# Performance work log

Measured on AMD Instinct MI355X. Metric: run time of the kernel, lower is better.

Reference implementation:

```python
import jax, jax.numpy as jnp
import numpy as np

S, B, D, H = 2048, 2, 1024, 16
DK = D // H


def setup_inputs() -> dict:
    key = jax.random.key(0)
    k1, k2, k3 = jax.random.split(key, 3)
    x = jax.random.normal(k1, (S, B, D), dtype=jnp.float32)
    # xavier-uniform-like scale for weights
    w_qkv = jax.random.normal(k2, (3 * D, D), dtype=jnp.float32) * (1.0 / np.sqrt(D))
    w_out = jax.random.normal(k3, (D, D), dtype=jnp.float32) * (1.0 / np.sqrt(D))
    b_out = jnp.zeros((D,), dtype=jnp.float32)
    return {"x": x, "w_qkv": w_qkv, "w_out": w_out, "b_out": b_out}


def reference(x, w_qkv, w_out, b_out):
    seq_len, batch, d_model = x.shape
    n_heads = H
    d_k = d_model // n_heads
    # qkv projection: [S,B,3D]
    qkv = jnp.einsum('sbd,ed->sbe', x, w_qkv)
    qkv = qkv.reshape(seq_len, batch, 3, n_heads, d_k)
    qkv = jnp.transpose(qkv, (2, 1, 3, 0, 4))  # [3,B,H,S,dk]
    q, k, v = qkv[0], qkv[1], qkv[2]
    scores = jnp.einsum('bhqd,bhkd->bhqk', q, k) / jnp.sqrt(jnp.asarray(d_k, x.dtype))
    causal = jnp.triu(jnp.ones((seq_len, seq_len), dtype=bool), k=1)
    scores = jnp.where(causal[None, None], jnp.asarray(-jnp.inf, scores.dtype), scores)
    weights = jax.nn.softmax(scores, axis=-1)
    out = jnp.einsum('bhqk,bhkd->bhqd', weights, v)  # [B,H,S,dk]
    out = jnp.transpose(out, (2, 0, 1, 3)).reshape(seq_len, batch, d_model)
    return jnp.einsum('sbd,ed->sbe', out, w_out) + b_out
```

## Files before the change

### kernel.cpp

```cpp
#include <hip/hip_runtime.h>
#include <cstdint>

typedef _Float16 f16;
typedef _Float16 f16x4 __attribute__((ext_vector_type(4)));
typedef _Float16 f16x8 __attribute__((ext_vector_type(8)));
typedef float f32x4 __attribute__((ext_vector_type(4)));

#define MFMA16(a, b, c) __builtin_amdgcn_mfma_f32_16x16x32_f16(a, b, c, 0, 0, 0)
#define QSCALE 0.1803368801111243f

__device__ __forceinline__ void gload_lds16(const void* g, void* l) {
    __builtin_amdgcn_global_load_lds((__attribute__((address_space(1))) void*)(g),
                                     (__attribute__((address_space(3))) void*)(l),
                                     16, 0, 0);
}


__global__ void cast_all(const float* __restrict__ x, const float* __restrict__ wqv,
                         const float* __restrict__ wo, f16* __restrict__ out) {
    int i = blockIdx.x * blockDim.x + threadIdx.x;
    const float* src; int li;
    if (i < 1048576)      { src = x;   li = i; }
    else if (i < 1835008) { src = wqv; li = i - 1048576; }
    else                  { src = wo;  li = i - 1835008; }
    float4 v = reinterpret_cast<const float4*>(src)[li];
    f16x4 o = {(f16)v.x, (f16)v.y, (f16)v.z, (f16)v.w};
    reinterpret_cast<f16x4*>(out)[i] = o;
}

__global__ __launch_bounds__(256) void gemm_qkv(
    const f16* __restrict__ A, const f16* __restrict__ B,
    f16* __restrict__ outq, f16* __restrict__ outk, f16* __restrict__ outvt)
{
    __shared__ f16 SM[128 * 64 * 2];
    f16* As = SM;
    f16* Bs = SM + 8192;
    const int tid = threadIdx.x;
    const int lane = tid & 63;
    const int wave = tid >> 6;
    const int wm = wave >> 1, wn = wave & 1;
    const int bm = blockIdx.y * 128, bn = blockIdx.x * 128;
    const int sr = tid >> 3;
    const int scu = (tid & 7) ^ (sr & 7);
    const int fr = lane & 15, fq = lane >> 4;
    const int u0 = (fq ^ (fr & 7)) * 8;
    const int u1 = ((4 + fq) ^ (fr & 7)) * 8;

    f32x4 acc[4][4] = {};

    for (int k0 = 0; k0 < 1024; k0 += 64) {
        __syncthreads();
#pragma unroll
        for (int is = 0; is < 4; ++is) {
            gload_lds16(&A[(bm + sr + is * 32) * 1024 + k0 + scu * 8], &As[is * 2048 + tid * 8]);
            gload_lds16(&B[(bn + sr + is * 32) * 1024 + k0 + scu * 8], &Bs[is * 2048 + tid * 8]);
        }
        __syncthreads();
        f16x8 af0[4], af1[4], bf0[4], bf1[4];
#pragma unroll
        for (int mt = 0; mt < 4; ++mt) {
            int r = wm * 64 + mt * 16 + fr;
            af0[mt] = *(const f16x8*)&As[r * 64 + u0];
            af1[mt] = *(const f16x8*)&As[r * 64 + u1];
        }
#pragma unroll
        for (int nt = 0; nt < 4; ++nt) {
            int r = wn * 64 + nt * 16 + fr;
            bf0[nt] = *(const f16x8*)&Bs[r * 64 + u0];
            bf1[nt] = *(const f16x8*)&Bs[r * 64 + u1];
        }
#pragma unroll
        for (int mt = 0; mt < 4; ++mt)
#pragma unroll
            for (int nt = 0; nt < 4; ++nt) {
                acc[mt][nt] = MFMA16(af0[mt], bf0[nt], acc[mt][nt]);
                acc[mt][nt] = MFMA16(af1[mt], bf1[nt], acc[mt][nt]);
            }
    }

    const int x = blockIdx.x;
    if (x < 16) {
        f16* base = (x < 8) ? outq : outk;
        const float scale = (x < 8) ? QSCALE : 1.0f;
        const int coloff = (x < 8) ? bn : (bn - 1024);
#pragma unroll
        for (int mt = 0; mt < 4; ++mt)
#pragma unroll
            for (int nt = 0; nt < 4; ++nt)
#pragma unroll
                for (int i = 0; i < 4; ++i) {
                    int row = bm + wm * 64 + mt * 16 + fq * 4 + i;
                    int col = coloff + wn * 64 + nt * 16 + fr;
                    int s = row >> 1, b = row & 1;
                    int h = col >> 6, dk = col & 63;
                    base[((b * 16 + h) * 2048 + s) * 64 + dk] = (f16)(acc[mt][nt][i] * scale);
                }
    } else {
        const int xb = x - 16;
        const int s0 = bm >> 1;
        f16* Ts = SM;
#pragma unroll
        for (int p = 0; p < 2; ++p) {
            __syncthreads();
            if (wn == p) {
#pragma unroll
                for (int mt = 0; mt < 4; ++mt)
#pragma unroll
                    for (int nt = 0; nt < 4; ++nt)
#pragma unroll
                        for (int i = 0; i < 4; ++i) {
                            int row = wm * 64 + mt * 16 + fq * 4 + i;
                            int cl = nt * 16 + fr;
                            Ts[(cl * 2 + (row & 1)) * 76 + (row >> 1)] = (f16)acc[mt][nt][i];
                        }
            }
            __syncthreads();
            const int h = xb * 2 + p;
            const int sj = tid & 7;
#pragma unroll
            for (int it = 0; it < 4; ++it) {
                int idx = (tid >> 3) + it * 32;
                int bsel = idx & 1, dk = idx >> 1;
                f16x8 v = *(const f16x8*)&Ts[(dk * 2 + bsel) * 76 + sj * 8];
                *(f16x8*)&outvt[((bsel * 16 + h) * 64 + dk) * 2048 + s0 + sj * 8] = v;
            }
        }
    }
}

__global__ __launch_bounds__(256) void attn_kernel(
    const f16* __restrict__ qg, const f16* __restrict__ kg,
    const f16* __restrict__ vtg, f16* __restrict__ attn)
{
    __shared__ f16 Ks[2][64 * 64];
    __shared__ f16 Vs[2][64 * 64];
    __shared__ f16 plds[4][16 * 72];
    const int tid = threadIdx.x;
    const int lane = tid & 63;
    const int wave = tid >> 6;
    const int qpair = blockIdx.x;
    const int bh = blockIdx.y;
    const int b = bh >> 4, h = bh & 15;
    const int fr = lane & 15, fq = lane >> 4;

    const int bqA = qpair * 64;
    const int bqB = (31 - qpair) * 64;
    const int nA = qpair + 1;
    const int nB = 32 - qpair;
    const int qrowA = bqA + wave * 16;
    const int qrowB = bqB + wave * 16;

    const f16* Q  = qg  + bh * 2048 * 64;
    const f16* K  = kg  + bh * 2048 * 64;
    const f16* VT = vtg + bh * 64 * 2048;
    f16* P = plds[wave];

    const int sr = tid >> 3;
    const int scu = (tid & 7) ^ (sr & 7);

    f16x8 aqA0 = *(const f16x8*)&Q[(qrowA + fr) * 64 + fq * 8];
    f16x8 aqA1 = *(const f16x8*)&Q[(qrowA + fr) * 64 + 32 + fq * 8];
    f16x8 aqB0 = *(const f16x8*)&Q[(qrowB + fr) * 64 + fq * 8];
    f16x8 aqB1 = *(const f16x8*)&Q[(qrowB + fr) * 64 + 32 + fq * 8];

    f32x4 oA[4] = {}, oB[4] = {};
    float lA[4] = {}, lB[4] = {};

    auto stage = [&](int kc, int buf) {
        const int kb = kc * 64;
        gload_lds16(&K[(kb + sr) * 64 + scu * 8],         &Ks[buf][tid * 8]);
        gload_lds16(&K[(kb + sr + 32) * 64 + scu * 8],    &Ks[buf][2048 + tid * 8]);
        gload_lds16(&VT[sr * 2048 + kb + scu * 8],        &Vs[buf][tid * 8]);
        gload_lds16(&VT[(sr + 32) * 2048 + kb + scu * 8], &Vs[buf][2048 + tid * 8]);
    };

    auto compute = [&](const f16x8& aq0, const f16x8& aq1, int qrow0, int kb,
                       const f16* Ksb, const f16* Vsb, f32x4* oacc, float* li, bool domask) {
        f32x4 sc[4] = {};
#pragma unroll
        for (int ct = 0; ct < 4; ++ct) {
            int r = ct * 16 + fr;
            f16x8 b0 = *(const f16x8*)&Ksb[r * 64 + ((fq ^ (r & 7)) * 8)];
            f16x8 b1 = *(const f16x8*)&Ksb[r * 64 + (((4 + fq) ^ (r & 7)) * 8)];
            sc[ct] = MFMA16(aq0, b0, sc[ct]);
            sc[ct] = MFMA16(aq1, b1, sc[ct]);
        }
        if (domask) {
#pragma unroll
            for (int ct = 0; ct < 4; ++ct) {
                int kcol = kb + ct * 16 + fr;
#pragma unroll
                for (int i = 0; i < 4; ++i)
                    if (kcol > qrow0 + fq * 4 + i) sc[ct][i] = -1e30f;
            }
        }
#pragma unroll
        for (int i = 0; i < 4; ++i) {
            float p0 = __builtin_amdgcn_exp2f(sc[0][i]);
            float p1 = __builtin_amdgcn_exp2f(sc[1][i]);
            float p2 = __builtin_amdgcn_exp2f(sc[2][i]);
            float p3 = __builtin_amdgcn_exp2f(sc[3][i]);
            li[i] += (p0 + p1) + (p2 + p3);
            P[(fq * 4 + i) * 72 + fr]      = (f16)p0;
            P[(fq * 4 + i) * 72 + 16 + fr] = (f16)p1;
            P[(fq * 4 + i) * 72 + 32 + fr] = (f16)p2;
            P[(fq * 4 + i) * 72 + 48 + fr] = (f16)p3;
        }
        f16x8 ap0 = *(const f16x8*)&P[fr * 72 + fq * 8];
        f16x8 ap1 = *(const f16x8*)&P[fr * 72 + 32 + fq * 8];
#pragma unroll
        for (int nt = 0; nt < 4; ++nt) {
            int dk = nt * 16 + fr;
            f16x8 bv0 = *(const f16x8*)&Vsb[dk * 64 + ((fq ^ (dk & 7)) * 8)];
            f16x8 bv1 = *(const f16x8*)&Vsb[dk * 64 + (((4 + fq) ^ (dk & 7)) * 8)];
            oacc[nt] = MFMA16(ap0, bv0, oacc[nt]);
            oacc[nt] = MFMA16(ap1, bv1, oacc[nt]);
        }
    };

    stage(0, 0);
    for (int kc = 0; kc < nB; ++kc) {
        const int kb = kc * 64;
        const int cur = kc & 1;
        __syncthreads();
        if (kc + 1 < nB) stage(kc + 1, cur ^ 1);
        compute(aqB0, aqB1, qrowB, kb, Ks[cur], Vs[cur], oB, lB, kb + 63 > qrowB);
        if (kc < nA)
            compute(aqA0, aqA1, qrowA, kb, Ks[cur], Vs[cur], oA, lA, kb + 63 > qrowA);
    }

#pragma unroll
    for (int i = 0; i < 4; ++i) {
        float rs = lA[i];
        rs += __shfl_xor(rs, 1);
        rs += __shfl_xor(rs, 2);
        rs += __shfl_xor(rs, 4);
        rs += __shfl_xor(rs, 8);
        float inv = __builtin_amdgcn_rcpf(rs);
        int srow = qrowA + fq * 4 + i;
#pragma unroll
        for (int nt = 0; nt < 4; ++nt)
            attn[(srow * 2 + b) * 1024 + h * 64 + nt * 16 + fr] = (f16)(oA[nt][i] * inv);
    }
#pragma unroll
    for (int i = 0; i < 4; ++i) {
        float rs = lB[i];
        rs += __shfl_xor(rs, 1);
        rs += __shfl_xor(rs, 2);
        rs += __shfl_xor(rs, 4);
        rs += __shfl_xor(rs, 8);
        float inv = __builtin_amdgcn_rcpf(rs);
        int srow = qrowB + fq * 4 + i;
#pragma unroll
        for (int nt = 0; nt < 4; ++nt)
            attn[(srow * 2 + b) * 1024 + h * 64 + nt * 16 + fr] = (f16)(oB[nt][i] * inv);
    }
}

__global__ __launch_bounds__(256) void gemm_out(
    const f16* __restrict__ A, const f16* __restrict__ B,
    const float* __restrict__ bias, float* __restrict__ out)
{
    __shared__ f16 As[128 * 64];
    __shared__ f16 Bs[64 * 64];
    const int tid = threadIdx.x;
    const int lane = tid & 63;
    const int wave = tid >> 6;
    const int wm = wave >> 1, wn = wave & 1;
    const int bm = blockIdx.y * 128, bn = blockIdx.x * 64;
    const int sr = tid >> 3;
    const int scu = (tid & 7) ^ (sr & 7);
    const int fr = lane & 15, fq = lane >> 4;
    const int u0 = (fq ^ (fr & 7)) * 8;
    const int u1 = ((4 + fq) ^ (fr & 7)) * 8;

    f32x4 acc[4][2] = {};

    for (int k0 = 0; k0 < 1024; k0 += 64) {
        __syncthreads();
#pragma unroll
        for (int is = 0; is < 4; ++is)
            gload_lds16(&A[(bm + sr + is * 32) * 1024 + k0 + scu * 8], &As[is * 2048 + tid * 8]);
#pragma unroll
        for (int is = 0; is < 2; ++is)
            gload_lds16(&B[(bn + sr + is * 32) * 1024 + k0 + scu * 8], &Bs[is * 2048 + tid * 8]);
        __syncthreads();
        f16x8 af0[4], af1[4], bf0[2], bf1[2];
#pragma unroll
        for (int mt = 0; mt < 4; ++mt) {
            int r = wm * 64 + mt * 16 + fr;
            af0[mt] = *(const f16x8*)&As[r * 64 + u0];
            af1[mt] = *(const f16x8*)&As[r * 64 + u1];
        }
#pragma unroll
        for (int nt = 0; nt < 2; ++nt) {
            int r = wn * 32 + nt * 16 + fr;
            bf0[nt] = *(const f16x8*)&Bs[r * 64 + u0];
            bf1[nt] = *(const f16x8*)&Bs[r * 64 + u1];
        }
#pragma unroll
        for (int mt = 0; mt < 4; ++mt)
#pragma unroll
            for (int nt = 0; nt < 2; ++nt) {
                acc[mt][nt] = MFMA16(af0[mt], bf0[nt], acc[mt][nt]);
                acc[mt][nt] = MFMA16(af1[mt], bf1[nt], acc[mt][nt]);
            }
    }

#pragma unroll
    for (int mt = 0; mt < 4; ++mt)
#pragma unroll
        for (int nt = 0; nt < 2; ++nt)
#pragma unroll
            for (int i = 0; i < 4; ++i) {
                int row = bm + wm * 64 + mt * 16 + fq * 4 + i;
                int col = bn + wn * 32 + nt * 16 + fr;
                out[row * 1024 + col] = acc[mt][nt][i] + bias[col];
            }
}

extern "C" void kernel_launch(void* const* d_in, const int* in_sizes, int n_in,
                              void* d_out, int out_size, void* d_ws, size_t ws_size,
                              hipStream_t stream)
{
    const float* x     = (const float*)d_in[0];
    const float* w_qkv = (const float*)d_in[1];
    const float* w_out = (const float*)d_in[2];
    const float* b_out = (const float*)d_in[3];
    float* out = (float*)d_out;

    char* ws = (char*)d_ws;
    f16* xh  = (f16*)(ws);
    f16* wqh = (f16*)(ws + 8388608);
    f16* woh = (f16*)(ws + 14680064);
    f16* qh  = (f16*)(ws + 16777216);
    f16* kh  = (f16*)(ws + 25165824);
    f16* vt  = (f16*)(ws + 33554432);
    f16* ah  = (f16*)(ws + 41943040);

    cast_all<<<8192, 256, 0, stream>>>(x, w_qkv, w_out, xh);
    gemm_qkv<<<dim3(24, 32), 256, 0, stream>>>(xh, wqh, qh, kh, vt);
    attn_kernel<<<dim3(16, 32), 256, 0, stream>>>(qh, kh, vt, ah);
    gemm_out<<<dim3(16, 32), 256, 0, stream>>>(ah, woh, b_out, out);
}
```

Measured before the change: 185.8 us.

## Split attention key range in two halves and merge with a combine kernel

The attention grid is doubled by splitting each query-pair's key loop into two halves. Each half writes unnormalized partial outputs and row sums to separate buffers in reused workspace. A new combine kernel then adds the partials and normalizes them. A constant table reorders block indices so the heavier halves are scheduled first. The aim is more parallelism and better load balance across CUs, at the cost of an extra kernel launch, extra global traffic, and unnormalized fp16 intermediates.

```diff
diff --git a/kernel.cpp b/kernel.cpp
--- a/kernel.cpp
+++ b/kernel.cpp
@@ -128,9 +128,14 @@
     }
 }
 
+__device__ __constant__ const unsigned char ATTN_ORDER[32] = {
+    18,20,22,14,16,10,12,24,26,6,8,2,4,28,30,0,
+    1,3,5,29,31,7,9,11,13,25,27,15,17,19,21,23};
+
 __global__ __launch_bounds__(256) void attn_kernel(
     const f16* __restrict__ qg, const f16* __restrict__ kg,
-    const f16* __restrict__ vtg, f16* __restrict__ attn)
+    const f16* __restrict__ vtg, f16* __restrict__ Op0, f16* __restrict__ Op1,
+    float* __restrict__ lp0, float* __restrict__ lp1)
 {
     __shared__ f16 Ks[2][64 * 64];
     __shared__ f16 Vs[2][64 * 64];
@@ -138,7 +143,9 @@
     const int tid = threadIdx.x;
     const int lane = tid & 63;
     const int wave = tid >> 6;
-    const int qpair = blockIdx.x;
+    const int enc = ATTN_ORDER[blockIdx.x];
+    const int qpair = enc >> 1;
+    const int half = enc & 1;
     const int bh = blockIdx.y;
     const int b = bh >> 4, h = bh & 15;
     const int fr = lane & 15, fq = lane >> 4;
@@ -147,6 +154,9 @@
     const int bqB = (31 - qpair) * 64;
     const int nA = qpair + 1;
     const int nB = 32 - qpair;
+    const int h0 = (nB + 1) >> 1;
+    const int k0 = half ? h0 : 0;
+    const int k1 = half ? nB : h0;
     const int qrowA = bqA + wave * 16;
     const int qrowB = bqB + wave * 16;
 
@@ -218,17 +228,19 @@
         }
     };
 
-    stage(0, 0);
-    for (int kc = 0; kc < nB; ++kc) {
+    stage(k0, k0 & 1);
+    for (int kc = k0; kc < k1; ++kc) {
         const int kb = kc * 64;
         const int cur = kc & 1;
         __syncthreads();
-        if (kc + 1 < nB) stage(kc + 1, cur ^ 1);
+        if (kc + 1 < k1) stage(kc + 1, cur ^ 1);
         compute(aqB0, aqB1, qrowB, kb, Ks[cur], Vs[cur], oB, lB, kb + 63 > qrowB);
         if (kc < nA)
             compute(aqA0, aqA1, qrowA, kb, Ks[cur], Vs[cur], oA, lA, kb + 63 > qrowA);
     }
 
+    f16* Op = half ? Op1 : Op0;
+    float* lp = half ? lp1 : lp0;
 #pragma unroll
     for (int i = 0; i < 4; ++i) {
         float rs = lA[i];
@@ -236,11 +248,11 @@
         rs += __shfl_xor(rs, 2);
         rs += __shfl_xor(rs, 4);
         rs += __shfl_xor(rs, 8);
-        float inv = __builtin_amdgcn_rcpf(rs);
         int srow = qrowA + fq * 4 + i;
+        if (fr == 0) lp[(srow * 2 + b) * 16 + h] = rs;
 #pragma unroll
         for (int nt = 0; nt < 4; ++nt)
-            attn[(srow * 2 + b) * 1024 + h * 64 + nt * 16 + fr] = (f16)(oA[nt][i] * inv);
+            Op[(srow * 2 + b) * 1024 + h * 64 + nt * 16 + fr] = (f16)oA[nt][i];
     }
 #pragma unroll
     for (int i = 0; i < 4; ++i) {
@@ -249,12 +261,28 @@
         rs += __shfl_xor(rs, 2);
         rs += __shfl_xor(rs, 4);
         rs += __shfl_xor(rs, 8);
-        float inv = __builtin_amdgcn_rcpf(rs);
         int srow = qrowB + fq * 4 + i;
+        if (fr == 0) lp[(srow * 2 + b) * 16 + h] = rs;
 #pragma unroll
         for (int nt = 0; nt < 4; ++nt)
-            attn[(srow * 2 + b) * 1024 + h * 64 + nt * 16 + fr] = (f16)(oB[nt][i] * inv);
-    }
+            Op[(srow * 2 + b) * 1024 + h * 64 + nt * 16 + fr] = (f16)oB[nt][i];
+    }
+}
+
+__global__ __launch_bounds__(256) void combine_kernel(
+    const f16* __restrict__ Op0, const float* __restrict__ lp0,
+    const float* __restrict__ lp1, f16* __restrict__ ah)
+{
+    const int idx = (blockIdx.x * 256 + threadIdx.x) * 8;
+    const int row = idx >> 10;
+    const int h = (idx >> 6) & 15;
+    float inv = __builtin_amdgcn_rcpf(lp0[row * 16 + h] + lp1[row * 16 + h]);
+    f16x8 a = *(const f16x8*)&Op0[idx];
+    f16x8 c = *(const f16x8*)&ah[idx];
+    f16x8 o;
+#pragma unroll
+    for (int j = 0; j < 8; ++j) o[j] = (f16)(((float)a[j] + (float)c[j]) * inv);
+    *(f16x8*)&ah[idx] = o;
 }
 
 __global__ __launch_bounds__(256) void gemm_out(
@@ -331,7 +359,10 @@
 
     char* ws = (char*)d_ws;
     f16* xh  = (f16*)(ws);
+    f16* Op0 = (f16*)(ws);
     f16* wqh = (f16*)(ws + 8388608);
+    float* lp0 = (float*)(ws + 8388608);
+    float* lp1 = (float*)(ws + 8388608 + 262144);
     f16* woh = (f16*)(ws + 14680064);
     f16* qh  = (f16*)(ws + 16777216);
     f16* kh  = (f16*)(ws + 25165824);
@@ -340,6 +371,7 @@
 
     cast_all<<<8192, 256, 0, stream>>>(x, w_qkv, w_out, xh);
     gemm_qkv<<<dim3(24, 32), 256, 0, stream>>>(xh, wqh, qh, kh, vt);
-    attn_kernel<<<dim3(16, 32), 256, 0, stream>>>(qh, kh, vt, ah);
+    attn_kernel<<<dim3(32, 32), 256, 0, stream>>>(qh, kh, vt, Op0, ah, lp0, lp1);
+    combine_kernel<<<2048, 256, 0, stream>>>(Op0, lp0, lp1, ah);
     gemm_out<<<dim3(16, 32), 256, 0, stream>>>(ah, woh, b_out, out);
 }
```

Result: slower. 196.1 us (+5.5%).

## Shrink output GEMM tile to 64x64 and use 32x32 MFMA

Applied to the files above, without the earlier changes.

The output projection GEMM drops from 128x64 to 64x64 tiles, doubling the grid to 1024 blocks. Each wave now computes a single 32x32 tile with the 32x32x16 MFMA instruction instead of a grid of 16x16 MFMAs, and the epilogue is rewritten for the 32x32 accumulator layout. The goal is more blocks to fill the GPU's compute units and fewer LDS fragment reads per MFMA. In exchange each block reuses its loaded data less, so global and LDS traffic per FLOP goes up.

```diff
diff --git a/kernel.cpp b/kernel.cpp
--- a/kernel.cpp
+++ b/kernel.cpp
@@ -5,8 +5,10 @@
 typedef _Float16 f16x4 __attribute__((ext_vector_type(4)));
 typedef _Float16 f16x8 __attribute__((ext_vector_type(8)));
 typedef float f32x4 __attribute__((ext_vector_type(4)));
+typedef float f32x16 __attribute__((ext_vector_type(16)));
 
 #define MFMA16(a, b, c) __builtin_amdgcn_mfma_f32_16x16x32_f16(a, b, c, 0, 0, 0)
+#define MFMA32(a, b, c) __builtin_amdgcn_mfma_f32_32x32x16_f16(a, b, c, 0, 0, 0)
 #define QSCALE 0.1803368801111243f
 
 __device__ __forceinline__ void gload_lds16(const void* g, void* l) {
@@ -261,62 +263,45 @@
     const f16* __restrict__ A, const f16* __restrict__ B,
     const float* __restrict__ bias, float* __restrict__ out)
 {
-    __shared__ f16 As[128 * 64];
+    __shared__ f16 As[64 * 64];
     __shared__ f16 Bs[64 * 64];
     const int tid = threadIdx.x;
     const int lane = tid & 63;
     const int wave = tid >> 6;
     const int wm = wave >> 1, wn = wave & 1;
-    const int bm = blockIdx.y * 128, bn = blockIdx.x * 64;
+    const int bm = blockIdx.y * 64, bn = blockIdx.x * 64;
     const int sr = tid >> 3;
     const int scu = (tid & 7) ^ (sr & 7);
-    const int fr = lane & 15, fq = lane >> 4;
-    const int u0 = (fq ^ (fr & 7)) * 8;
-    const int u1 = ((4 + fq) ^ (fr & 7)) * 8;
-
-    f32x4 acc[4][2] = {};
+    const int col = lane & 31;
+    const int H = lane >> 5;
+
+    f32x16 acc = {};
 
     for (int k0 = 0; k0 < 1024; k0 += 64) {
         __syncthreads();
 #pragma unroll
-        for (int is = 0; is < 4; ++is)
+        for (int is = 0; is < 2; ++is) {
             gload_lds16(&A[(bm + sr + is * 32) * 1024 + k0 + scu * 8], &As[is * 2048 + tid * 8]);
-#pragma unroll
-        for (int is = 0; is < 2; ++is)
             gload_lds16(&B[(bn + sr + is * 32) * 1024 + k0 + scu * 8], &Bs[is * 2048 + tid * 8]);
-        __syncthreads();
-        f16x8 af0[4], af1[4], bf0[2], bf1[2];
-#pragma unroll
-        for (int mt = 0; mt < 4; ++mt) {
-            int r = wm * 64 + mt * 16 + fr;
-            af0[mt] = *(const f16x8*)&As[r * 64 + u0];
-            af1[mt] = *(const f16x8*)&As[r * 64 + u1];
-        }
-#pragma unroll
-        for (int nt = 0; nt < 2; ++nt) {
-            int r = wn * 32 + nt * 16 + fr;
-            bf0[nt] = *(const f16x8*)&Bs[r * 64 + u0];
-            bf1[nt] = *(const f16x8*)&Bs[r * 64 + u1];
-        }
-#pragma unroll
-        for (int mt = 0; mt < 4; ++mt)
-#pragma unroll
-            for (int nt = 0; nt < 2; ++nt) {
-                acc[mt][nt] = MFMA16(af0[mt], bf0[nt], acc[mt][nt]);
-                acc[mt][nt] = MFMA16(af1[mt], bf1[nt], acc[mt][nt]);
-            }
-    }
-
-#pragma unroll
-    for (int mt = 0; mt < 4; ++mt)
-#pragma unroll
-        for (int nt = 0; nt < 2; ++nt)
-#pragma unroll
-            for (int i = 0; i < 4; ++i) {
-                int row = bm + wm * 64 + mt * 16 + fq * 4 + i;
-                int col = bn + wn * 32 + nt * 16 + fr;
-                out[row * 1024 + col] = acc[mt][nt][i] + bias[col];
-            }
+        }
+        __syncthreads();
+        const int ra = wm * 32 + col;
+        const int rb = wn * 32 + col;
+#pragma unroll
+        for (int c = 0; c < 4; ++c) {
+            f16x8 af = *(const f16x8*)&As[ra * 64 + (((c * 2 + H) ^ (ra & 7)) * 8)];
+            f16x8 bf = *(const f16x8*)&Bs[rb * 64 + (((c * 2 + H) ^ (rb & 7)) * 8)];
+            acc = MFMA32(af, bf, acc);
+        }
+    }
+
+    const int ocol = bn + wn * 32 + col;
+    const float bv = bias[ocol];
+#pragma unroll
+    for (int g = 0; g < 16; ++g) {
+        int row = bm + wm * 32 + (g & 3) + 8 * (g >> 2) + 4 * H;
+        out[row * 1024 + ocol] = acc[g] + bv;
+    }
 }
 
 extern "C" void kernel_launch(void* const* d_in, const int* in_sizes, int n_in,
@@ -341,5 +326,5 @@
     cast_all<<<8192, 256, 0, stream>>>(x, w_qkv, w_out, xh);
     gemm_qkv<<<dim3(24, 32), 256, 0, stream>>>(xh, wqh, qh, kh, vt);
     attn_kernel<<<dim3(16, 32), 256, 0, stream>>>(qh, kh, vt, ah);
-    gemm_out<<<dim3(16, 32), 256, 0, stream>>>(ah, woh, b_out, out);
-}
+    gemm_out<<<dim3(16, 64), 256, 0, stream>>>(ah, woh, b_out, out);
+}
```

After: 189.6 us. +2.1%, slower.
